# Kernel tuning notes

Hardware: AMD Instinct MI355X
Metric: run time of the kernel (lower is better)

The kernel has to match this reference:

```python
import jax, jax.numpy as jnp
import numpy as np

_SAMPLING_EPS = 1e-5
BIG_NEG = jnp.float32(-1e30)  # finite stand-in for -inf (exact 0 after softmax in fp32)


def setup_inputs() -> dict:
    key = jax.random.key(0)
    ks = jax.random.split(key, 12)
    B, V, P, O, S = 128, 128000, 2048, 256, 4
    return {
        "logits": jax.random.normal(ks[0], (B, V), jnp.float32) * 4.0,
        "prompt_token_ids": jax.random.randint(ks[1], (B, P), 0, V),
        "output_token_ids": jax.random.randint(ks[2], (B, O), 0, V),
        "stop_token_ids": jax.random.randint(ks[3], (B, S), 0, V),
        "min_tokens": jax.random.randint(ks[4], (B,), 0, 512),
        "presence_penalties": jax.random.uniform(ks[5], (B,), jnp.float32),
        "frequency_penalties": jax.random.uniform(ks[6], (B,), jnp.float32),
        "repetition_penalties": 1.0 + 0.3 * jax.random.uniform(ks[7], (B,), jnp.float32),
        "temperature": 0.5 + jax.random.uniform(ks[8], (B,), jnp.float32),
        "top_k": jax.random.randint(ks[9], (B,), 32, 64),
        "top_p": 0.5 + 0.5 * jax.random.uniform(ks[10], (B,), jnp.float32),
        "uniform_noise": jax.random.uniform(ks[11], (B, V), jnp.float32, minval=1e-10, maxval=1.0),
        "max_num_logprobs": 20,
    }


def reference(logits, prompt_token_ids, output_token_ids, stop_token_ids,
              min_tokens, presence_penalties, frequency_penalties,
              repetition_penalties, temperature, top_k, top_p,
              uniform_noise, max_num_logprobs):
    B, V = logits.shape
    x = logits.astype(jnp.float32)
    rows = jnp.arange(B)[:, None]

    # ---- min-token penalty: set stop-token logits to -inf while len(output) < min_tokens
    need = min_tokens > output_token_ids.shape[1]                  # [B]
    stop_pen = jnp.where(need[:, None], BIG_NEG, jnp.inf)          # [B,S]
    x = x.at[rows, stop_token_ids].min(stop_pen)

    # ---- presence / frequency / repetition penalties (vLLM apply_penalties)
    counts = jnp.zeros((B, V), jnp.float32).at[rows, output_token_ids].add(1.0)
    prompt_mask = jnp.zeros((B, V), bool).at[rows, prompt_token_ids].set(True)
    output_mask = counts > 0
    rp = repetition_penalties[:, None]
    penalized = jnp.where(x > 0, x / rp, x * rp)
    x = jnp.where(prompt_mask | output_mask, penalized, x)
    x = x - frequency_penalties[:, None] * counts \
          - presence_penalties[:, None] * output_mask.astype(jnp.float32)

    # ---- temperature (greedy rows: temp treated as 1.0)
    t = jnp.where(temperature < _SAMPLING_EPS, 1.0, temperature)
    x = x / t[:, None]

    # ---- top-k / top-p filtering (per-row k and p)
    order = jnp.argsort(-x, axis=-1)                               # descending
    srt = jnp.take_along_axis(x, order, axis=-1)
    pos = jnp.arange(V)[None, :]
    k_eff = jnp.where(top_k < 1, V, top_k)
    keep_k = pos < k_eff[:, None]
    probs_s = jax.nn.softmax(srt, axis=-1)
    cum = jnp.cumsum(probs_s, axis=-1)
    keep_p = (cum - probs_s) < top_p[:, None]                      # cumulative mass before token < p
    keep = jnp.zeros((B, V), bool).at[rows, order].set(keep_k & keep_p)
    x = jnp.where(keep, x, BIG_NEG)

    orig_logits = x
    # source applies temperature a second time before the final sample
    x2 = x / t[:, None]

    # ---- sample: Gumbel-max random sampling, greedy where temperature ~ 0
    gumbel = -jnp.log(-jnp.log(uniform_noise))
    random_sampled = jnp.argmax(x2 + gumbel, axis=-1)
    greedy_sampled = jnp.argmax(x2, axis=-1)
    sampled = jnp.where(temperature < _SAMPLING_EPS, greedy_sampled,
                        random_sampled).astype(jnp.int32)

    # ---- top-k logprobs
    logprobs = jax.nn.log_softmax(orig_logits, axis=-1)
    topk_logprobs, topk_indices = jax.lax.top_k(logprobs, max_num_logprobs)
    return sampled, topk_logprobs, topk_indices.astype(jnp.int32)
```

## Files before the change

kernel.cpp:

```cpp
#include <hip/hip_runtime.h>
#include <math.h>

#define VV 128000
#define NB 128
#define PP 2048
#define OO 256

#define S   10
#define CH  12800
#define CW  400
#define NT1 256
#define CAP 256
#define HS1 512

#define NT2 256
#define MC  1024

#define BIG_NEG_F (-1e30f)
#define PAD_KEY 0x007FFFFF80000000ULL
#define LOG2E 1.4426950408889634f

__device__ __forceinline__ unsigned long long packkey(float f, int idx) {
  unsigned int b = __float_as_uint(f);
  unsigned int mf = (b & 0x80000000u) ? ~b : (b | 0x80000000u);
  return ((unsigned long long)mf << 32) | (unsigned long long)(unsigned int)(~(unsigned int)idx);
}
__device__ __forceinline__ float unpack_val(unsigned long long k) {
  unsigned int mf = (unsigned int)(k >> 32);
  unsigned int b = (mf & 0x80000000u) ? (mf & 0x7fffffffu) : ~mf;
  return __uint_as_float(b);
}
__device__ __forceinline__ int unpack_idx(unsigned long long k) {
  return (int)(~(unsigned int)(k & 0xffffffffu));
}
__device__ __forceinline__ float ulp_down(float f, int n) {
  unsigned int b = __float_as_uint(f);
  unsigned int m = (b & 0x80000000u) ? ~b : (b | 0x80000000u);
  m -= (unsigned int)n;
  unsigned int r = (m & 0x80000000u) ? (m & 0x7fffffffu) : ~m;
  return __uint_as_float(r);
}

template <int N, int T>
__device__ __forceinline__ void bitonic_desc_u64(unsigned long long* a, int tid) {
  for (int k = 2; k <= N; k <<= 1) {
    for (int j = k >> 1; j > 0; j >>= 1) {
      for (int i = tid; i < N; i += T) {
        int ixj = i ^ j;
        if (ixj > i) {
          unsigned long long x = a[i], y = a[ixj];
          bool up = (i & k) == 0;
          if ((x < y) == up) { a[i] = y; a[ixj] = x; }
        }
      }
      __syncthreads();
    }
  }
}

template <int N, int T>
__device__ __forceinline__ void bitonic_desc_f32(float* a, int tid) {
  for (int k = 2; k <= N; k <<= 1) {
    for (int j = k >> 1; j > 0; j >>= 1) {
      for (int i = tid; i < N; i += T) {
        int ixj = i ^ j;
        if (ixj > i) {
          float x = a[i], y = a[ixj];
          bool up = (i & k) == 0;
          if ((x < y) == up) { a[i] = y; a[ixj] = x; }
        }
      }
      __syncthreads();
    }
  }
}

__global__ __launch_bounds__(NT1)
void k1_select(const float* __restrict__ logits,
               const int* __restrict__ prompt_ids,
               const int* __restrict__ output_ids,
               const int* __restrict__ stop_ids,
               const int* __restrict__ min_tokens,
               const float* __restrict__ presence_p,
               const float* __restrict__ frequency_p,
               const float* __restrict__ repetition_p,
               const float* __restrict__ temperature,
               unsigned long long* __restrict__ ws_cand,
               float* __restrict__ ws_sum)
{
#pragma clang fp contract(off)
  __shared__ unsigned int pbits[CW];
  __shared__ unsigned int obits[CW];
  __shared__ int hkey[HS1];
  __shared__ int hval[HS1];
  __shared__ float tmax[NT1];
  __shared__ unsigned long long cand[CAP];
  __shared__ float wsum[NT1 / 64];
  __shared__ int cnt_sh;

  const int chunk = blockIdx.x;
  const int row   = blockIdx.y;
  const int tid   = threadIdx.x;
  const int base  = chunk * CH;

  const float fp  = frequency_p[row];
  const float pp  = presence_p[row];
  const float rp  = repetition_p[row];
  const float inv_rp = 1.0f / rp;
  const float tmp = temperature[row];
  const float t   = (tmp < 1e-5f) ? 1.0f : tmp;
  const float c2  = LOG2E / t;
  const bool need = min_tokens[row] > OO;
  const int s0 = stop_ids[row * 4 + 0];
  const int s1 = stop_ids[row * 4 + 1];
  const int s2 = stop_ids[row * 4 + 2];
  const int s3 = stop_ids[row * 4 + 3];
  const bool anystop = need &&
      (((unsigned)(s0 - base) < CH) || ((unsigned)(s1 - base) < CH) ||
       ((unsigned)(s2 - base) < CH) || ((unsigned)(s3 - base) < CH));

  for (int i = tid; i < CW; i += NT1) { pbits[i] = 0u; obits[i] = 0u; }
  for (int i = tid; i < HS1; i += NT1) { hkey[i] = -1; hval[i] = 0; }
  if (tid == 0) cnt_sh = 0;
  __syncthreads();

  for (int i = tid; i < PP; i += NT1) {
    int tok = prompt_ids[row * PP + i];
    int l = tok - base;
    if ((unsigned)l < CH) atomicOr(&pbits[l >> 5], 1u << (l & 31));
  }
  for (int i = tid; i < OO; i += NT1) {
    int tok = output_ids[row * OO + i];
    int l = tok - base;
    if ((unsigned)l < CH) {
      atomicOr(&obits[l >> 5], 1u << (l & 31));
      unsigned int h = ((unsigned int)tok * 2654435761u) >> 23;
      for (;;) {
        int k = hkey[h];
        if (k == tok) { atomicAdd(&hval[h], 1); break; }
        if (k == -1) {
          int prev = atomicCAS(&hkey[h], -1, tok);
          if (prev == -1 || prev == tok) { atomicAdd(&hval[h], 1); break; }
          continue;
        }
        h = (h + 1) & (HS1 - 1);
      }
    }
  }
  __syncthreads();

  const float* __restrict__ lrow = logits + (size_t)row * VV + base;

  float mx = -INFINITY;
  float esum = 0.0f;
  for (int it = 0; it < (CH + NT1 * 4 - 1) / (NT1 * 4); ++it) {
    int li = (it * NT1 + tid) << 2;
    if (li >= CH) break;
    float4 xv = *(const float4*)(lrow + li);
    unsigned int w  = (unsigned)li >> 5;
    unsigned int sh = (unsigned)li & 31u;
    unsigned int pm4 = (pbits[w] >> sh) & 15u;
    unsigned int om4 = (obits[w] >> sh) & 15u;
#pragma unroll
    for (int e = 0; e < 4; ++e) {
      float x = (&xv.x)[e];
      int v = base + li + e;
      float xp = x;
      if (anystop && ((v == s0) | (v == s1) | (v == s2) | (v == s3)))
        xp = BIG_NEG_F;
      if ((pm4 | om4) & (1u << e)) {
        xp = (xp > 0.0f) ? (xp * inv_rp) : (xp * rp);
        if ((om4 >> e) & 1u) {
          float cnt = 0.0f;
          unsigned int h = ((unsigned int)v * 2654435761u) >> 23;
          for (;;) {
            int k = hkey[h];
            if (k == -1) break;
            if (k == v) { cnt = (float)hval[h]; break; }
            h = (h + 1) & (HS1 - 1);
          }
          xp = xp - fp * cnt - pp;
        }
      }
      mx = fmaxf(mx, xp);
      esum += exp2f(xp * c2);
    }
  }

  float s = esum;
#pragma unroll
  for (int off = 32; off > 0; off >>= 1) s += __shfl_down(s, off, 64);
  if ((tid & 63) == 0) wsum[tid >> 6] = s;

  tmax[tid] = mx;
  __syncthreads();
  bitonic_desc_f32<NT1, NT1>(tmax, tid);
  const float tau = ulp_down(tmax[63], 8);
  __syncthreads();

  for (int it = 0; it < (CH + NT1 * 4 - 1) / (NT1 * 4); ++it) {
    int li = (it * NT1 + tid) << 2;
    if (li >= CH) break;
    float4 xv = *(const float4*)(lrow + li);
#pragma unroll
    for (int e = 0; e < 4; ++e) {
      float x = (&xv.x)[e];
      if (x >= tau) {
        int v = base + li + e;
        if (anystop && ((v == s0) | (v == s1) | (v == s2) | (v == s3)))
          x = fminf(x, BIG_NEG_F);
        unsigned int w  = (unsigned)(li + e) >> 5;
        unsigned int sh = (unsigned)(li + e) & 31u;
        bool pm = (pbits[w] >> sh) & 1u;
        bool om = (obits[w] >> sh) & 1u;
        float cnt = 0.0f;
        if (om) {
          unsigned int h = ((unsigned int)v * 2654435761u) >> 23;
          for (;;) {
            int k = hkey[h];
            if (k == -1) break;
            if (k == v) { cnt = (float)hval[h]; break; }
            h = (h + 1) & (HS1 - 1);
          }
        }
        if (pm || om) x = (x > 0.0f) ? (x / rp) : (x * rp);
        x = x - fp * cnt;
        if (om) x = x - pp;
        if (x >= tau) {
          float xd = x / t;
          int p = atomicAdd(&cnt_sh, 1);
          if (p < CAP) cand[p] = packkey(xd, v);
        }
      }
    }
  }
  __syncthreads();
  int total = cnt_sh; if (total > CAP) total = CAP;
  for (int i = tid; i < CAP; i += NT1)
    if (i >= total) cand[i] = PAD_KEY;
  __syncthreads();

  bitonic_desc_u64<CAP, NT1>(cand, tid);

  if (tid < 64) ws_cand[((size_t)row * S + chunk) * 64 + tid] = cand[tid];
  if (tid == 0) ws_sum[row * S + chunk] = wsum[0] + wsum[1] + wsum[2] + wsum[3];
}

__global__ __launch_bounds__(NT2)
void k2_finalize(const float* __restrict__ temperature,
                 const int* __restrict__ top_k,
                 const float* __restrict__ top_p,
                 const float* __restrict__ noise,
                 const unsigned long long* __restrict__ ws_cand,
                 const float* __restrict__ ws_sum,
                 float* __restrict__ out, int K)
{
#pragma clang fp contract(off)
  __shared__ unsigned long long cand[MC];
  __shared__ float sv[64];
  __shared__ int   si[64];
  __shared__ float se[64];
  __shared__ float gv[64];

  const int row = blockIdx.x;
  const int tid = threadIdx.x;

  const float tmp = temperature[row];
  const float t   = (tmp < 1e-5f) ? 1.0f : tmp;
  const int   tk  = top_k[row];
  const float tpv = top_p[row];

  for (int i = tid; i < MC; i += NT2)
    cand[i] = (i < S * 64) ? ws_cand[(size_t)row * S * 64 + i] : PAD_KEY;
  __syncthreads();

  bitonic_desc_u64<MC, NT2>(cand, tid);

  if (tid < 64) {
    unsigned long long kk = cand[tid];
    float val = unpack_val(kk);
    int   idx = unpack_idx(kk);
    float m = unpack_val(cand[0]);
    sv[tid] = val;
    si[tid] = idx;
    bool ok = (unsigned)idx < VV;
    float u = ok ? noise[(size_t)row * VV + idx] : 0.5f;
    float g = -logf(-logf(u));
    se[tid] = expf(val - m);
    gv[tid] = val / t + g;
  }
  __syncthreads();

  if (tid == 0) {
    float Ssum = 0.0f;
    for (int c = 0; c < S; c++) Ssum += ws_sum[row * S + c];
    const float m = sv[0];
    const float Z = Ssum * exp2f(-m * LOG2E);

    int keff = (tk < 1) ? 64 : (tk < 64 ? tk : 64);

    float cum = 0.0f;
    int nk = 0;
    for (int j = 0; j < 64; j++) {
      if (j >= keff) break;
      if (!(cum < tpv)) break;
      nk++;
      cum += se[j] / Z;
    }

    float Zk = 0.0f;
    for (int j = 0; j < nk; j++) Zk += se[j];
    const float logZk = logf(Zk);

    float bv = -INFINITY; int bi = 0x7fffffff;
    for (int j = 0; j < nk; j++) {
      float val = gv[j];
      if (val > bv || (val == bv && si[j] < bi)) { bv = val; bi = si[j]; }
    }
    const int samp = (tmp < 1e-5f) ? si[0] : bi;
    out[row] = (float)samp;

    unsigned long long bm0 = 0ull, bm1 = 0ull;
    for (int j = 0; j < nk; j++) {
      int ix = si[j];
      if (ix < 64) bm0 |= 1ull << ix;
      else if (ix < 128) bm1 |= 1ull << (ix - 64);
    }
    int fi = 0;
    for (int j = 0; j < K; j++) {
      float lp; int ix;
      if (j < nk) {
        lp = (sv[j] - m) - logZk;
        ix = si[j];
      } else {
        while ((fi < 64) ? ((bm0 >> fi) & 1ull) : ((bm1 >> (fi - 64)) & 1ull)) fi++;
        ix = fi; fi++;
        lp = BIG_NEG_F;
      }
      out[NB + row * K + j]            = lp;
      out[NB + NB * K + row * K + j]   = (float)ix;
    }
  }
}

extern "C" void kernel_launch(void* const* d_in, const int* in_sizes, int n_in,
                              void* d_out, int out_size, void* d_ws, size_t ws_size,
                              hipStream_t stream) {
  const float* logits = (const float*)d_in[0];
  const int*   prompt = (const int*)d_in[1];
  const int*   outids = (const int*)d_in[2];
  const int*   stop   = (const int*)d_in[3];
  const int*   mint   = (const int*)d_in[4];
  const float* pres   = (const float*)d_in[5];
  const float* freq   = (const float*)d_in[6];
  const float* rep    = (const float*)d_in[7];
  const float* temp   = (const float*)d_in[8];
  const int*   topk   = (const int*)d_in[9];
  const float* topp   = (const float*)d_in[10];
  const float* noise  = (const float*)d_in[11];

  int B_ = in_sizes[4];
  int K_ = (out_size - B_) / (2 * B_);

  unsigned long long* ws_cand = (unsigned long long*)d_ws;
  float* ws_sum = (float*)(ws_cand + (size_t)NB * S * 64);

  dim3 g1(S, B_);
  k1_select<<<g1, NT1, 0, stream>>>(logits, prompt, outids, stop, mint,
                                    pres, freq, rep, temp, ws_cand, ws_sum);
  k2_finalize<<<B_, NT2, 0, stream>>>(temp, topk, topp, noise,
                                      ws_cand, ws_sum, (float*)d_out, K_);
}
```

Before: 224.9 us.

## Replace per-chunk shared sorts with wave sorts and direct candidate spill

```diff
diff --git a/kernel.cpp b/kernel.cpp
--- a/kernel.cpp
+++ b/kernel.cpp
@@ -6,15 +6,15 @@
 #define PP 2048
 #define OO 256
 
-#define S   10
-#define CH  12800
-#define CW  400
+#define S   8
+#define CH  16000
+#define CW  500
 #define NT1 256
-#define CAP 256
+#define CAP 128
 #define HS1 512
 
 #define NT2 256
-#define MC  1024
+#define MC  (S*CAP)
 
 #define BIG_NEG_F (-1e30f)
 #define PAD_KEY 0x007FFFFF80000000ULL
@@ -39,6 +39,19 @@
   m -= (unsigned int)n;
   unsigned int r = (m & 0x80000000u) ? (m & 0x7fffffffu) : ~m;
   return __uint_as_float(r);
+}
+
+__device__ __forceinline__ float wave_sort64_desc(float v, int lane) {
+  for (int k = 2; k <= 64; k <<= 1) {
+    for (int j = k >> 1; j > 0; j >>= 1) {
+      float o = __shfl_xor(v, j, 64);
+      bool smaller = (lane & j) == 0;
+      bool dir = (lane & k) == 0;
+      bool keepmax = (smaller == dir);
+      v = keepmax ? fmaxf(v, o) : fminf(v, o);
+    }
+  }
+  return v;
 }
 
 template <int N, int T>
@@ -58,23 +71,6 @@
   }
 }
 
-template <int N, int T>
-__device__ __forceinline__ void bitonic_desc_f32(float* a, int tid) {
-  for (int k = 2; k <= N; k <<= 1) {
-    for (int j = k >> 1; j > 0; j >>= 1) {
-      for (int i = tid; i < N; i += T) {
-        int ixj = i ^ j;
-        if (ixj > i) {
-          float x = a[i], y = a[ixj];
-          bool up = (i & k) == 0;
-          if ((x < y) == up) { a[i] = y; a[ixj] = x; }
-        }
-      }
-      __syncthreads();
-    }
-  }
-}
-
 __global__ __launch_bounds__(NT1)
 void k1_select(const float* __restrict__ logits,
                const int* __restrict__ prompt_ids,
@@ -86,21 +82,23 @@
                const float* __restrict__ repetition_p,
                const float* __restrict__ temperature,
                unsigned long long* __restrict__ ws_cand,
-               float* __restrict__ ws_sum)
+               float* __restrict__ ws_sum,
+               int* __restrict__ ws_cnt)
 {
 #pragma clang fp contract(off)
   __shared__ unsigned int pbits[CW];
   __shared__ unsigned int obits[CW];
   __shared__ int hkey[HS1];
   __shared__ int hval[HS1];
-  __shared__ float tmax[NT1];
-  __shared__ unsigned long long cand[CAP];
+  __shared__ float smax[NT1];
   __shared__ float wsum[NT1 / 64];
+  __shared__ float tau_sh;
   __shared__ int cnt_sh;
 
   const int chunk = blockIdx.x;
   const int row   = blockIdx.y;
   const int tid   = threadIdx.x;
+  const int lane  = tid & 63;
   const int base  = chunk * CH;
 
   const float fp  = frequency_p[row];
@@ -124,10 +122,14 @@
   if (tid == 0) cnt_sh = 0;
   __syncthreads();
 
-  for (int i = tid; i < PP; i += NT1) {
-    int tok = prompt_ids[row * PP + i];
-    int l = tok - base;
-    if ((unsigned)l < CH) atomicOr(&pbits[l >> 5], 1u << (l & 31));
+  const int4* pr4 = (const int4*)(prompt_ids + (size_t)row * PP);
+  for (int i = tid; i < PP / 4; i += NT1) {
+    int4 tv = pr4[i];
+    int l;
+    l = tv.x - base; if ((unsigned)l < CH) atomicOr(&pbits[l >> 5], 1u << (l & 31));
+    l = tv.y - base; if ((unsigned)l < CH) atomicOr(&pbits[l >> 5], 1u << (l & 31));
+    l = tv.z - base; if ((unsigned)l < CH) atomicOr(&pbits[l >> 5], 1u << (l & 31));
+    l = tv.w - base; if ((unsigned)l < CH) atomicOr(&pbits[l >> 5], 1u << (l & 31));
   }
   for (int i = tid; i < OO; i += NT1) {
     int tok = output_ids[row * OO + i];
@@ -150,100 +152,115 @@
   __syncthreads();
 
   const float* __restrict__ lrow = logits + (size_t)row * VV + base;
+  const int NIT = (CH + NT1 * 8 - 1) / (NT1 * 8);
 
   float mx = -INFINITY;
   float esum = 0.0f;
-  for (int it = 0; it < (CH + NT1 * 4 - 1) / (NT1 * 4); ++it) {
-    int li = (it * NT1 + tid) << 2;
-    if (li >= CH) break;
-    float4 xv = *(const float4*)(lrow + li);
-    unsigned int w  = (unsigned)li >> 5;
-    unsigned int sh = (unsigned)li & 31u;
-    unsigned int pm4 = (pbits[w] >> sh) & 15u;
-    unsigned int om4 = (obits[w] >> sh) & 15u;
+  for (int it = 0; it < NIT; ++it) {
+    int li = (it * NT1 + tid) << 3;
+    if (li < CH) {
+      float4 xa = *(const float4*)(lrow + li);
+      float4 xb = *(const float4*)(lrow + li + 4);
+      unsigned int w  = (unsigned)li >> 5;
+      unsigned int sh = (unsigned)li & 31u;
+      unsigned int pm8 = (pbits[w] >> sh) & 255u;
+      unsigned int om8 = (obits[w] >> sh) & 255u;
+      float xs[8] = {xa.x, xa.y, xa.z, xa.w, xb.x, xb.y, xb.z, xb.w};
 #pragma unroll
-    for (int e = 0; e < 4; ++e) {
-      float x = (&xv.x)[e];
-      int v = base + li + e;
-      float xp = x;
-      if (anystop && ((v == s0) | (v == s1) | (v == s2) | (v == s3)))
-        xp = BIG_NEG_F;
-      if ((pm4 | om4) & (1u << e)) {
-        xp = (xp > 0.0f) ? (xp * inv_rp) : (xp * rp);
-        if ((om4 >> e) & 1u) {
+      for (int e = 0; e < 8; ++e) {
+        float xp = xs[e];
+        int v = base + li + e;
+        if (anystop && ((v == s0) | (v == s1) | (v == s2) | (v == s3)))
+          xp = BIG_NEG_F;
+        if ((pm8 | om8) & (1u << e)) {
+          xp = (xp > 0.0f) ? (xp * inv_rp) : (xp * rp);
+          if ((om8 >> e) & 1u) {
+            float cnt = 0.0f;
+            unsigned int h = ((unsigned int)v * 2654435761u) >> 23;
+            for (;;) {
+              int k = hkey[h];
+              if (k == -1) break;
+              if (k == v) { cnt = (float)hval[h]; break; }
+              h = (h + 1) & (HS1 - 1);
+            }
+            xp = xp - fp * cnt - pp;
+          }
+        }
+        mx = fmaxf(mx, xp);
+        esum += exp2f(xp * c2);
+      }
+    }
+  }
+
+  float ss = esum;
+#pragma unroll
+  for (int off = 32; off > 0; off >>= 1) ss += __shfl_down(ss, off, 64);
+  if (lane == 0) wsum[tid >> 6] = ss;
+
+  smax[tid] = wave_sort64_desc(mx, lane);
+  __syncthreads();
+
+  if (tid == 0) {
+    int p0 = 0, p1 = 0, p2 = 0, p3 = 0;
+    float tau = -INFINITY;
+    for (int n = 0; n < 64; ++n) {
+      float v0 = (p0 < 64) ? smax[p0]       : -INFINITY;
+      float v1 = (p1 < 64) ? smax[64 + p1]  : -INFINITY;
+      float v2 = (p2 < 64) ? smax[128 + p2] : -INFINITY;
+      float v3 = (p3 < 64) ? smax[192 + p3] : -INFINITY;
+      float m01 = fmaxf(v0, v1), m23 = fmaxf(v2, v3);
+      float m = fmaxf(m01, m23);
+      if (m == v0) p0++;
+      else if (m == v1) p1++;
+      else if (m == v2) p2++;
+      else p3++;
+      tau = m;
+    }
+    tau_sh = ulp_down(tau, 16);
+    ws_sum[row * S + chunk] = wsum[0] + wsum[1] + wsum[2] + wsum[3];
+  }
+  __syncthreads();
+  const float taueff = tau_sh;
+
+  unsigned long long* __restrict__ wc = ws_cand + ((size_t)row * S + chunk) * CAP;
+  for (int it = 0; it < NIT; ++it) {
+    int li = (it * NT1 + tid) << 3;
+    if (li < CH) {
+      float4 xa = *(const float4*)(lrow + li);
+      float4 xb = *(const float4*)(lrow + li + 4);
+      float xs[8] = {xa.x, xa.y, xa.z, xa.w, xb.x, xb.y, xb.z, xb.w};
+#pragma unroll
+      for (int e = 0; e < 8; ++e) {
+        float x = xs[e];
+        if (x >= taueff) {
+          int v = base + li + e;
+          int ll = li + e;
+          if (anystop && ((v == s0) | (v == s1) | (v == s2) | (v == s3)))
+            x = fminf(x, BIG_NEG_F);
+          bool pm = (pbits[(unsigned)ll >> 5] >> ((unsigned)ll & 31u)) & 1u;
+          bool om = (obits[(unsigned)ll >> 5] >> ((unsigned)ll & 31u)) & 1u;
           float cnt = 0.0f;
-          unsigned int h = ((unsigned int)v * 2654435761u) >> 23;
-          for (;;) {
-            int k = hkey[h];
-            if (k == -1) break;
-            if (k == v) { cnt = (float)hval[h]; break; }
-            h = (h + 1) & (HS1 - 1);
+          if (om) {
+            unsigned int h = ((unsigned int)v * 2654435761u) >> 23;
+            for (;;) {
+              int k = hkey[h];
+              if (k == -1) break;
+              if (k == v) { cnt = (float)hval[h]; break; }
+              h = (h + 1) & (HS1 - 1);
+            }
           }
-          xp = xp - fp * cnt - pp;
+          if (pm || om) x = (x > 0.0f) ? (x / rp) : (x * rp);
+          x = x - fp * cnt;
+          if (om) x = x - pp;
+          float xd = x / t;
+          int p = atomicAdd(&cnt_sh, 1);
+          if (p < CAP) wc[p] = packkey(xd, v);
         }
       }
-      mx = fmaxf(mx, xp);
-      esum += exp2f(xp * c2);
-    }
-  }
-
-  float s = esum;
-#pragma unroll
-  for (int off = 32; off > 0; off >>= 1) s += __shfl_down(s, off, 64);
-  if ((tid & 63) == 0) wsum[tid >> 6] = s;
-
-  tmax[tid] = mx;
-  __syncthreads();
-  bitonic_desc_f32<NT1, NT1>(tmax, tid);
-  const float tau = ulp_down(tmax[63], 8);
-  __syncthreads();
-
-  for (int it = 0; it < (CH + NT1 * 4 - 1) / (NT1 * 4); ++it) {
-    int li = (it * NT1 + tid) << 2;
-    if (li >= CH) break;
-    float4 xv = *(const float4*)(lrow + li);
-#pragma unroll
-    for (int e = 0; e < 4; ++e) {
-      float x = (&xv.x)[e];
-      if (x >= tau) {
-        int v = base + li + e;
-        if (anystop && ((v == s0) | (v == s1) | (v == s2) | (v == s3)))
-          x = fminf(x, BIG_NEG_F);
-        unsigned int w  = (unsigned)(li + e) >> 5;
-        unsigned int sh = (unsigned)(li + e) & 31u;
-        bool pm = (pbits[w] >> sh) & 1u;
-        bool om = (obits[w] >> sh) & 1u;
-        float cnt = 0.0f;
-        if (om) {
-          unsigned int h = ((unsigned int)v * 2654435761u) >> 23;
-          for (;;) {
-            int k = hkey[h];
-            if (k == -1) break;
-            if (k == v) { cnt = (float)hval[h]; break; }
-            h = (h + 1) & (HS1 - 1);
-          }
-        }
-        if (pm || om) x = (x > 0.0f) ? (x / rp) : (x * rp);
-        x = x - fp * cnt;
-        if (om) x = x - pp;
-        if (x >= tau) {
-          float xd = x / t;
-          int p = atomicAdd(&cnt_sh, 1);
-          if (p < CAP) cand[p] = packkey(xd, v);
-        }
-      }
-    }
-  }
-  __syncthreads();
-  int total = cnt_sh; if (total > CAP) total = CAP;
-  for (int i = tid; i < CAP; i += NT1)
-    if (i >= total) cand[i] = PAD_KEY;
-  __syncthreads();
-
-  bitonic_desc_u64<CAP, NT1>(cand, tid);
-
-  if (tid < 64) ws_cand[((size_t)row * S + chunk) * 64 + tid] = cand[tid];
-  if (tid == 0) ws_sum[row * S + chunk] = wsum[0] + wsum[1] + wsum[2] + wsum[3];
+    }
+  }
+  __syncthreads();
+  if (tid == 0) ws_cnt[row * S + chunk] = (cnt_sh < CAP) ? cnt_sh : CAP;
 }
 
 __global__ __launch_bounds__(NT2)
@@ -253,10 +270,12 @@
                  const float* __restrict__ noise,
                  const unsigned long long* __restrict__ ws_cand,
                  const float* __restrict__ ws_sum,
+                 const int* __restrict__ ws_cnt,
                  float* __restrict__ out, int K)
 {
 #pragma clang fp contract(off)
   __shared__ unsigned long long cand[MC];
+  __shared__ int cnts[S];
   __shared__ float sv[64];
   __shared__ int   si[64];
   __shared__ float se[64];
@@ -270,8 +289,14 @@
   const int   tk  = top_k[row];
   const float tpv = top_p[row];
 
-  for (int i = tid; i < MC; i += NT2)
-    cand[i] = (i < S * 64) ? ws_cand[(size_t)row * S * 64 + i] : PAD_KEY;
+  if (tid < S) cnts[tid] = ws_cnt[row * S + tid];
+  __syncthreads();
+
+  for (int g = tid; g < MC; g += NT2) {
+    int c = g >> 7;
+    int i = g & (CAP - 1);
+    cand[g] = (i < cnts[c]) ? ws_cand[((size_t)row * S + c) * CAP + i] : PAD_KEY;
+  }
   __syncthreads();
 
   bitonic_desc_u64<MC, NT2>(cand, tid);
@@ -363,11 +388,14 @@
   int K_ = (out_size - B_) / (2 * B_);
 
   unsigned long long* ws_cand = (unsigned long long*)d_ws;
-  float* ws_sum = (float*)(ws_cand + (size_t)NB * S * 64);
+  float* ws_sum = (float*)(ws_cand + (size_t)NB * S * CAP);
+  int*   ws_cnt = (int*)(ws_sum + (size_t)NB * S);
 
   dim3 g1(S, B_);
   k1_select<<<g1, NT1, 0, stream>>>(logits, prompt, outids, stop, mint,
-                                    pres, freq, rep, temp, ws_cand, ws_sum);
+                                    pres, freq, rep, temp,
+                                    ws_cand, ws_sum, ws_cnt);
   k2_finalize<<<B_, NT2, 0, stream>>>(temp, topk, topp, noise,
-                                      ws_cand, ws_sum, (float*)d_out, K_);
-}
+                                      ws_cand, ws_sum, ws_cnt,
+                                      (float*)d_out, K_);
+}
```

After: 226.3 us. Within noise of the previous version (+0.6%).
